# Kernel optimization log

Measured on AMD Instinct MI355X. Metric: run time of the kernel, lower is better.

## Reference

```python
import jax, jax.numpy as jnp
import numpy as np

# Model dims (see init_kwargs): embed_dim=64, heads=8, d_k = n_wires = 8
V, D, H, NQ, L, FFN = 32000, 64, 8, 8, 2, 128
B, S = 16, 1024
LAT, H1, H2, NC = 32, 128, 64, 10
INV_SQRT_DK = 1.0 / float(np.sqrt(NQ))
LN_EPS = 1e-5


def _pos_encoding(s, d):
    pos = jnp.arange(s, dtype=jnp.float32)[:, None]
    div = jnp.exp(jnp.arange(0, d, 2, dtype=jnp.float32) * (-np.log(10000.0) / d))
    pe = jnp.zeros((s, d), dtype=jnp.float32)
    pe = pe.at[:, 0::2].set(jnp.sin(pos * div))
    pe = pe.at[:, 1::2].set(jnp.cos(pos * div))
    return pe


def _layernorm(x, g, b):
    mu = jnp.mean(x, axis=-1, keepdims=True)
    var = jnp.mean(jnp.square(x - mu), axis=-1, keepdims=True)
    return (x - mu) * jax.lax.rsqrt(var + LN_EPS) * g + b


def _quantum_heads(x, theta):
    # Analytic simulation of the per-head 8-qubit VQC:
    #   RX(x_i) RX(theta_i) on wire i, CNOT ring (0->1..6->7, 7->0), measure Z.
    # Heisenberg picture: <Z_j> = prod_{i=0..j} cos(x_i+theta_i) for j>=1,
    # <Z_0> = prod_{i=1..7} cos(x_i+theta_i).
    b, s, _ = x.shape
    a = x.reshape(b, s, H, NQ) + theta            # [B,S,H,NQ]
    c = jnp.cos(a)
    cp = jnp.cumprod(c, axis=-1)
    z0 = jnp.prod(c[..., 1:], axis=-1, keepdims=True)
    return jnp.concatenate([z0, cp[..., 1:]], axis=-1)  # [B,S,H,NQ]


def _quantum_attention(x, theta, combine_W):
    qkv = _quantum_heads(x, theta)                 # [B,S,H,dk]
    q = qkv.transpose(0, 2, 1, 3)                  # [B,H,S,dk]
    scores = jnp.einsum('bhqd,bhkd->bhqk', q, q) * INV_SQRT_DK
    p = jax.nn.softmax(scores, axis=-1)
    out = jnp.einsum('bhqk,bhkd->bhqd', p, q)
    out = out.transpose(0, 2, 1, 3).reshape(x.shape[0], x.shape[1], D)
    return out @ combine_W.T                       # no bias (use_bias=False)


def _quantum_ffn(x, theta, W1, b1, W2, b2):
    # FFN QLayer: RX(x_i) then RY(theta_i), no entanglement -> <Z_i> = cos(theta_i)*cos(x_i)
    # GeneralEncoder only reads the first NQ features of each token.
    z = jnp.cos(x[..., :NQ]) * jnp.cos(theta)      # [B,S,NQ]
    h = jax.nn.relu(z @ W1.T + b1)                 # linear1 then ReLU
    return h @ W2.T + b2                           # linear2


def _forward(tokens, emb_table, attn_theta, combine_W, ln1_g, ln1_b, ln2_g, ln2_b,
             ffn_theta, ffn_W1, ffn_b1, ffn_W2, ffn_b2,
             enc_W1, enc_b1, enc_W2, enc_b2, enc_W3, enc_b3,
             dec_W1, dec_b1, dec_W2, dec_b2, dec_W3, dec_b3, cls_W, cls_b):
    x = emb_table[tokens] + _pos_encoding(tokens.shape[1], D)  # embed + positional
    for l in range(L):  # fixed small number of structurally distinct blocks
        a = _quantum_attention(x, attn_theta[l], combine_W[l])
        x = _layernorm(x + a, ln1_g[l], ln1_b[l])
        f = _quantum_ffn(x, ffn_theta[l], ffn_W1[l], ffn_b1[l], ffn_W2[l], ffn_b2[l])
        x = _layernorm(x + f, ln2_g[l], ln2_b[l])
    pooled = jnp.mean(x, axis=1)                   # [B,D]
    # AutoencoderQuantumNet.forward = decode(encode(x)) (quantum_ffn unused there)
    h = jax.nn.relu(pooled @ enc_W1.T + enc_b1)
    h = jax.nn.relu(h @ enc_W2.T + enc_b2)
    lat = h @ enc_W3.T + enc_b3
    h = jax.nn.relu(lat @ dec_W1.T + dec_b1)
    h = jax.nn.relu(h @ dec_W2.T + dec_b2)
    rec = h @ dec_W3.T + dec_b3                    # [B,D]
    return rec @ cls_W.T + cls_b                   # [B,NC]


def setup_inputs() -> dict:
    key = jax.random.key(0)
    ks = list(jax.random.split(key, 32))
    it = iter(ks)
    def nrm(shape, scale=0.05):
        return (jax.random.normal(next(it), shape) * scale).astype(jnp.float32)
    return {
        'tokens': jax.random.randint(next(it), (B, S), 0, V),
        'emb_table': nrm((V, D), 0.02),
        'attn_theta': nrm((L, NQ), 0.1),
        'combine_W': nrm((L, D, D)),
        'ln1_g': jnp.ones((L, D), jnp.float32), 'ln1_b': jnp.zeros((L, D), jnp.float32),
        'ln2_g': jnp.ones((L, D), jnp.float32), 'ln2_b': jnp.zeros((L, D), jnp.float32),
        'ffn_theta': nrm((L, NQ), 0.1),
        'ffn_W1': nrm((L, FFN, NQ)), 'ffn_b1': jnp.zeros((L, FFN), jnp.float32),
        'ffn_W2': nrm((L, D, FFN)), 'ffn_b2': jnp.zeros((L, D), jnp.float32),
        'enc_W1': nrm((H1, D)), 'enc_b1': jnp.zeros((H1,), jnp.float32),
        'enc_W2': nrm((H2, H1)), 'enc_b2': jnp.zeros((H2,), jnp.float32),
        'enc_W3': nrm((LAT, H2)), 'enc_b3': jnp.zeros((LAT,), jnp.float32),
        'dec_W1': nrm((H2, LAT)), 'dec_b1': jnp.zeros((H2,), jnp.float32),
        'dec_W2': nrm((H1, H2)), 'dec_b2': jnp.zeros((H1,), jnp.float32),
        'dec_W3': nrm((D, H1)), 'dec_b3': jnp.zeros((D,), jnp.float32),
        'cls_W': nrm((NC, D)), 'cls_b': jnp.zeros((NC,), jnp.float32),
    }


def reference(tokens, emb_table, attn_theta, combine_W, ln1_g, ln1_b, ln2_g, ln2_b,
              ffn_theta, ffn_W1, ffn_b1, ffn_W2, ffn_b2,
              enc_W1, enc_b1, enc_W2, enc_b2, enc_W3, enc_b3,
              dec_W1, dec_b1, dec_W2, dec_b2, dec_W3, dec_b3, cls_W, cls_b):
    return _forward(tokens, emb_table, attn_theta, combine_W, ln1_g, ln1_b, ln2_g, ln2_b,
                    ffn_theta, ffn_W1, ffn_b1, ffn_W2, ffn_b2,
                    enc_W1, enc_b1, enc_W2, enc_b2, enc_W3, enc_b3,
                    dec_W1, dec_b1, dec_W2, dec_b2, dec_W3, dec_b3, cls_W, cls_b)
```

## Files before the change

### kernel.cpp

```cpp
#include <hip/hip_runtime.h>
#include <math.h>

typedef _Float16 h2 __attribute__((ext_vector_type(2)));
typedef __fp16 hh4 __attribute__((ext_vector_type(4)));
typedef float f4 __attribute__((ext_vector_type(4)));

#define Bsz 16
#define Ssz 1024
#define TOKENS (Bsz * Ssz)
#define Dd 64
#define Hh 8
#define QTTS 520

#if __has_builtin(__builtin_amdgcn_exp2f)
  #define EXPFN(x) __builtin_amdgcn_exp2f(x)
  #define SQRT_PRESCALE 0.7141921f
#else
  #define EXPFN(x) __expf(x)
  #define SQRT_PRESCALE 0.5946036f
#endif

#if __has_builtin(__builtin_amdgcn_mfma_f32_16x16x16_f16)
  #define MFMA16(a, b, c) __builtin_amdgcn_mfma_f32_16x16x16_f16(a, b, c, 0, 0, 0)
#else
  #define MFMA16(a, b, c) __builtin_amdgcn_mfma_f32_16x16x16f16(a, b, c, 0, 0, 0)
#endif

__device__ __forceinline__ h2 pkrtz(float a, float b) {
#if __has_builtin(__builtin_amdgcn_cvt_pkrtz)
  return __builtin_bit_cast(h2, __builtin_amdgcn_cvt_pkrtz(a, b));
#else
  h2 r; r.x = (_Float16)a; r.y = (_Float16)b; return r;
#endif
}
__device__ __forceinline__ unsigned int as_u32(h2 v) {
  return __builtin_bit_cast(unsigned int, v);
}
__device__ __forceinline__ hh4 bc4(uint2 u) {
  return __builtin_bit_cast(hh4, u);
}

#if __has_builtin(__builtin_amdgcn_readlane)
__device__ __forceinline__ float rdlane(float v, int l) {
  return __int_as_float(__builtin_amdgcn_readlane(__float_as_int(v), l));
}
#else
__device__ __forceinline__ float rdlane(float v, int l) { return __shfl(v, l, 64); }
#endif

__device__ __forceinline__ void qheads(const float* __restrict__ xp,
                                       const float* th, float* o) {
  float4 v0 = *(const float4*)(xp);
  float4 v1 = *(const float4*)(xp + 4);
  float c0 = __cosf(v0.x + th[0]), c1 = __cosf(v0.y + th[1]);
  float c2 = __cosf(v0.z + th[2]), c3 = __cosf(v0.w + th[3]);
  float c4 = __cosf(v1.x + th[4]), c5 = __cosf(v1.y + th[5]);
  float c6 = __cosf(v1.z + th[6]), c7 = __cosf(v1.w + th[7]);
  float cp = c0;
  cp *= c1; o[1] = cp; cp *= c2; o[2] = cp; cp *= c3; o[3] = cp;
  cp *= c4; o[4] = cp; cp *= c5; o[5] = cp; cp *= c6; o[6] = cp;
  cp *= c7; o[7] = cp;
  o[0] = c1 * c2 * c3 * c4 * c5 * c6 * c7;
}

__global__ __launch_bounds__(256) void embed_kernel(
    const int* __restrict__ tokens, const float* __restrict__ emb,
    float* __restrict__ x) {
  int gid = blockIdx.x * 256 + threadIdx.x;
  if (gid >= TOKENS * 32) return;
  int d2 = gid & 31;
  int ts = gid >> 5;
  int s  = ts & (Ssz - 1);
  int tok = tokens[ts];
  float freq = __expf((float)(2 * d2) * (-0.14391156831f));
  float ang = (float)s * freq;
  float sn, cs;
  __sincosf(ang, &sn, &cs);
  float2 e2 = *(const float2*)&emb[(size_t)tok * Dd + 2 * d2];
  float2 r;
  r.x = e2.x + sn;
  r.y = e2.y + cs;
  *(float2*)&x[(size_t)ts * Dd + 2 * d2] = r;
}

__global__ __launch_bounds__(256, 4) void attn_kernel(
    const float* __restrict__ x, const float* __restrict__ theta,
    float* __restrict__ o_out, float* __restrict__ ps_out) {
  __shared__ unsigned int qrs[Ssz * 4 + 2];
  __shared__ unsigned int qtt[8 * QTTS];
  int blk = blockIdx.x;
  int bh = blk >> 3, split = blk & 7;
  int b = bh >> 3, h = bh & 7;
  int t = threadIdx.x;

  float th[8];
#pragma unroll
  for (int i = 0; i < 8; i++) th[i] = theta[i];

  const float* xb = x + (size_t)b * Ssz * Dd + h * 8;

#pragma unroll
  for (int i = 0; i < 4; i += 2) {
    int k0 = t * 4 + i;
    float oa[8], ob[8];
    qheads(xb + (size_t)k0 * Dd, th, oa);
    qheads(xb + (size_t)(k0 + 1) * Dd, th, ob);
    uint4 wa, wb;
    wa.x = as_u32(pkrtz(oa[0] * SQRT_PRESCALE, oa[1] * SQRT_PRESCALE));
    wa.y = as_u32(pkrtz(oa[2] * SQRT_PRESCALE, oa[3] * SQRT_PRESCALE));
    wa.z = as_u32(pkrtz(oa[4] * SQRT_PRESCALE, oa[5] * SQRT_PRESCALE));
    wa.w = as_u32(pkrtz(oa[6] * SQRT_PRESCALE, oa[7] * SQRT_PRESCALE));
    wb.x = as_u32(pkrtz(ob[0] * SQRT_PRESCALE, ob[1] * SQRT_PRESCALE));
    wb.y = as_u32(pkrtz(ob[2] * SQRT_PRESCALE, ob[3] * SQRT_PRESCALE));
    wb.z = as_u32(pkrtz(ob[4] * SQRT_PRESCALE, ob[5] * SQRT_PRESCALE));
    wb.w = as_u32(pkrtz(ob[6] * SQRT_PRESCALE, ob[7] * SQRT_PRESCALE));
    *(uint4*)&qrs[k0 * 4] = wa;
    *(uint4*)&qrs[(k0 + 1) * 4] = wb;
#pragma unroll
    for (int d = 0; d < 8; d++)
      qtt[d * QTTS + (k0 >> 1)] = as_u32(pkrtz(oa[d], ob[d]));
  }
  if (t == 0) { qrs[Ssz * 4] = 0; qrs[Ssz * 4 + 1] = 0; }
  __syncthreads();

  int l = t & 63, w = t >> 6;
  int g = l >> 4, rr = l & 15;
  int rt0 = split * 8 + w * 2;
  int rowA = rt0 * 16 + rr;
  int rowB = rowA + 16;
  uint2 z2; z2.x = 0; z2.y = 0;
  uint2 buA = (g < 2) ? *(const uint2*)&qrs[rowA * 4 + 2 * g] : z2;
  uint2 buB = (g < 2) ? *(const uint2*)&qrs[rowB * 4 + 2 * g] : z2;
  hh4 BrA = bc4(buA), BrB = bc4(buB);
  int aoff  = (g < 2) ? (rr * 4 + 2 * g) : (Ssz * 4);
  int astep = (g < 2) ? 64 : 0;
  int qoff  = (rr & 7) * QTTS + 2 * g;
  f4 zf = {0.f, 0.f, 0.f, 0.f};
  f4 accA0 = zf, accB0 = zf, accA1 = zf, accB1 = zf;
  float psA0 = 0.f, psB0 = 0.f, psA1 = 0.f, psB1 = 0.f;

#pragma unroll 4
  for (int kt = 0; kt < 64; kt += 2) {
    {
      uint2 au = *(const uint2*)&qrs[aoff + kt * astep];
      hh4 Ak = bc4(au);
      f4 sA = MFMA16(Ak, BrA, zf);
      f4 sB = MFMA16(Ak, BrB, zf);
      float pA0 = EXPFN(sA.x), pA1 = EXPFN(sA.y), pA2 = EXPFN(sA.z), pA3 = EXPFN(sA.w);
      float pB0 = EXPFN(sB.x), pB1 = EXPFN(sB.y), pB2 = EXPFN(sB.z), pB3 = EXPFN(sB.w);
      psA0 += (pA0 + pA1) + (pA2 + pA3);
      psB0 += (pB0 + pB1) + (pB2 + pB3);
      uint2 pbA, pbB;
      pbA.x = as_u32(pkrtz(pA0, pA1)); pbA.y = as_u32(pkrtz(pA2, pA3));
      pbB.x = as_u32(pkrtz(pB0, pB1)); pbB.y = as_u32(pkrtz(pB2, pB3));
      uint2 qt = *(const uint2*)&qtt[qoff + kt * 8];
      hh4 Aq = bc4(qt);
      accA0 = MFMA16(Aq, bc4(pbA), accA0);
      accB0 = MFMA16(Aq, bc4(pbB), accB0);
    }
    {
      uint2 au = *(const uint2*)&qrs[aoff + (kt + 1) * astep];
      hh4 Ak = bc4(au);
      f4 sA = MFMA16(Ak, BrA, zf);
      f4 sB = MFMA16(Ak, BrB, zf);
      float pA0 = EXPFN(sA.x), pA1 = EXPFN(sA.y), pA2 = EXPFN(sA.z), pA3 = EXPFN(sA.w);
      float pB0 = EXPFN(sB.x), pB1 = EXPFN(sB.y), pB2 = EXPFN(sB.z), pB3 = EXPFN(sB.w);
      psA1 += (pA0 + pA1) + (pA2 + pA3);
      psB1 += (pB0 + pB1) + (pB2 + pB3);
      uint2 pbA, pbB;
      pbA.x = as_u32(pkrtz(pA0, pA1)); pbA.y = as_u32(pkrtz(pA2, pA3));
      pbB.x = as_u32(pkrtz(pB0, pB1)); pbB.y = as_u32(pkrtz(pB2, pB3));
      uint2 qt = *(const uint2*)&qtt[qoff + (kt + 1) * 8];
      hh4 Aq = bc4(qt);
      accA1 = MFMA16(Aq, bc4(pbA), accA1);
      accB1 = MFMA16(Aq, bc4(pbB), accB1);
    }
  }
  f4 accA = accA0 + accA1;
  f4 accB = accB0 + accB1;
  float psA = psA0 + psA1, psB = psB0 + psB1;
  psA += __shfl_xor(psA, 16, 64); psA += __shfl_xor(psA, 32, 64);
  psB += __shfl_xor(psB, 16, 64); psB += __shfl_xor(psB, 32, 64);

  size_t tokA = (size_t)b * Ssz + rowA;
  size_t tokB = (size_t)b * Ssz + rowB;
  if (g < 2) {
    *(f4*)&o_out[tokA * 64 + h * 8 + 4 * g] = accA;
    *(f4*)&o_out[tokB * 64 + h * 8 + 4 * g] = accB;
  }
  if (l < 16) {
    ps_out[tokA * 8 + h] = psA;
    ps_out[tokB * 8 + h] = psB;
  }
}

__global__ __launch_bounds__(64) void tail1_kernel(
    float* __restrict__ x, const float* __restrict__ o_out,
    const float* __restrict__ ps_out, const float* __restrict__ Wc,
    const float* __restrict__ g1, const float* __restrict__ bb1) {
  int l = threadIdx.x & 63;
  int g = l >> 4, c = l & 15;
  int tok0 = blockIdx.x * 16;

  hh4 Bf[4][4];
#pragma unroll
  for (int dc = 0; dc < 4; dc++)
#pragma unroll
    for (int kc = 0; kc < 4; kc++) {
      float4 wv = *(const float4*)&Wc[(size_t)(dc * 16 + c) * 64 + kc * 16 + 4 * g];
      uint2 u; u.x = as_u32(pkrtz(wv.x, wv.y)); u.y = as_u32(pkrtz(wv.z, wv.w));
      Bf[kc][dc] = bc4(u);
    }

  int tka = tok0 + c;
  hh4 Af[4];
#pragma unroll
  for (int kc = 0; kc < 4; kc++) {
    float4 o4 = *(const float4*)&o_out[(size_t)tka * 64 + kc * 16 + 4 * g];
    float inv = 1.0f / ps_out[(size_t)tka * 8 + kc * 2 + (g >> 1)];
    uint2 u;
    u.x = as_u32(pkrtz(o4.x * inv, o4.y * inv));
    u.y = as_u32(pkrtz(o4.z * inv, o4.w * inv));
    Af[kc] = bc4(u);
  }

  f4 zf = {0.f, 0.f, 0.f, 0.f};
  float yy[4][4];
#pragma unroll
  for (int dc = 0; dc < 4; dc++) {
    f4 acc = zf;
#pragma unroll
    for (int kc = 0; kc < 4; kc++) acc = MFMA16(Af[kc], Bf[kc][dc], acc);
    yy[dc][0] = acc.x; yy[dc][1] = acc.y; yy[dc][2] = acc.z; yy[dc][3] = acc.w;
  }

  float g1v[4], b1v[4];
#pragma unroll
  for (int dc = 0; dc < 4; dc++) { g1v[dc] = g1[dc * 16 + c]; b1v[dc] = bb1[dc * 16 + c]; }

#pragma unroll
  for (int r = 0; r < 4; r++) {
    int tok = tok0 + 4 * g + r;
    float rv0 = x[(size_t)tok * 64 + c]      + yy[0][r];
    float rv1 = x[(size_t)tok * 64 + 16 + c] + yy[1][r];
    float rv2 = x[(size_t)tok * 64 + 32 + c] + yy[2][r];
    float rv3 = x[(size_t)tok * 64 + 48 + c] + yy[3][r];
    float s = (rv0 + rv1) + (rv2 + rv3);
    s += __shfl_xor(s, 1, 64); s += __shfl_xor(s, 2, 64);
    s += __shfl_xor(s, 4, 64); s += __shfl_xor(s, 8, 64);
    float mu = s * (1.f / 64.f);
    float t0 = rv0 - mu, t1 = rv1 - mu, t2 = rv2 - mu, t3 = rv3 - mu;
    float q = (t0 * t0 + t1 * t1) + (t2 * t2 + t3 * t3);
    q += __shfl_xor(q, 1, 64); q += __shfl_xor(q, 2, 64);
    q += __shfl_xor(q, 4, 64); q += __shfl_xor(q, 8, 64);
    float inv = rsqrtf(q * (1.f / 64.f) + 1e-5f);
    x[(size_t)tok * 64 + c]      = t0 * inv * g1v[0] + b1v[0];
    x[(size_t)tok * 64 + 16 + c] = t1 * inv * g1v[1] + b1v[1];
    x[(size_t)tok * 64 + 32 + c] = t2 * inv * g1v[2] + b1v[2];
    x[(size_t)tok * 64 + 48 + c] = t3 * inv * g1v[3] + b1v[3];
  }
}

__global__ __launch_bounds__(64) void tail2_kernel(
    float* __restrict__ x,
    const float* __restrict__ g2, const float* __restrict__ bb2,
    const float* __restrict__ fth,
    const float* __restrict__ W1, const float* __restrict__ fb1,
    const float* __restrict__ W2, const float* __restrict__ fb2,
    float* __restrict__ partial, int do_partial) {
  int l = threadIdx.x & 63;
  int g = l >> 4, c = l & 15;
  int tok0 = blockIdx.x * 16;

  float4 x4[4];
#pragma unroll
  for (int dc = 0; dc < 4; dc++)
    x4[dc] = *(const float4*)&x[(size_t)(tok0 + c) * 64 + dc * 16 + 4 * g];

  uint2 uz; uz.x = 0; uz.y = 0;
  if (g < 2) {
    float4 thv = *(const float4*)&fth[4 * g];
    float z0 = __cosf(x4[0].x) * __cosf(thv.x);
    float z1 = __cosf(x4[0].y) * __cosf(thv.y);
    float z2 = __cosf(x4[0].z) * __cosf(thv.z);
    float z3 = __cosf(x4[0].w) * __cosf(thv.w);
    uz.x = as_u32(pkrtz(z0, z1)); uz.y = as_u32(pkrtz(z2, z3));
  }
  hh4 Bz = bc4(uz);

  f4 zf = {0.f, 0.f, 0.f, 0.f};

  hh4 Bh[8];
#pragma unroll
  for (int jc = 0; jc < 8; jc++) {
    uint2 uw; uw.x = 0; uw.y = 0;
    if (g < 2) {
      float4 wv = *(const float4*)&W1[(size_t)(jc * 16 + c) * 8 + 4 * g];
      uw.x = as_u32(pkrtz(wv.x, wv.y)); uw.y = as_u32(pkrtz(wv.z, wv.w));
    }
    f4 d1 = MFMA16(bc4(uw), Bz, zf);
    float4 b1v = *(const float4*)&fb1[jc * 16 + 4 * g];
    float h0 = fmaxf(d1.x + b1v.x, 0.f);
    float h1 = fmaxf(d1.y + b1v.y, 0.f);
    float h2 = fmaxf(d1.z + b1v.z, 0.f);
    float h3 = fmaxf(d1.w + b1v.w, 0.f);
    uint2 uh;
    uh.x = as_u32(pkrtz(h0, h1)); uh.y = as_u32(pkrtz(h2, h3));
    Bh[jc] = bc4(uh);
  }

  float ff[4][4];
#pragma unroll
  for (int dc = 0; dc < 4; dc++) {
    f4 acc = zf;
#pragma unroll
    for (int kc = 0; kc < 8; kc++) {
      float4 wv = *(const float4*)&W2[(size_t)(dc * 16 + c) * 128 + kc * 16 + 4 * g];
      uint2 uw;
      uw.x = as_u32(pkrtz(wv.x, wv.y)); uw.y = as_u32(pkrtz(wv.z, wv.w));
      acc = MFMA16(bc4(uw), Bh[kc], acc);
    }
    ff[dc][0] = acc.x; ff[dc][1] = acc.y; ff[dc][2] = acc.z; ff[dc][3] = acc.w;
  }

  float r2[4][4];
  float s = 0.f;
#pragma unroll
  for (int dc = 0; dc < 4; dc++) {
    float4 b2v = *(const float4*)&fb2[dc * 16 + 4 * g];
    r2[dc][0] = x4[dc].x + ff[dc][0] + b2v.x;
    r2[dc][1] = x4[dc].y + ff[dc][1] + b2v.y;
    r2[dc][2] = x4[dc].z + ff[dc][2] + b2v.z;
    r2[dc][3] = x4[dc].w + ff[dc][3] + b2v.w;
    s += (r2[dc][0] + r2[dc][1]) + (r2[dc][2] + r2[dc][3]);
  }
  s += __shfl_xor(s, 16, 64); s += __shfl_xor(s, 32, 64);
  float mu = s * (1.f / 64.f);
  float q = 0.f;
#pragma unroll
  for (int dc = 0; dc < 4; dc++) {
#pragma unroll
    for (int r = 0; r < 4; r++) { r2[dc][r] -= mu; q += r2[dc][r] * r2[dc][r]; }
  }
  q += __shfl_xor(q, 16, 64); q += __shfl_xor(q, 32, 64);
  float inv = rsqrtf(q * (1.f / 64.f) + 1e-5f);

  float xo[4][4];
#pragma unroll
  for (int dc = 0; dc < 4; dc++) {
    float4 gv = *(const float4*)&g2[dc * 16 + 4 * g];
    float4 bv = *(const float4*)&bb2[dc * 16 + 4 * g];
    xo[dc][0] = r2[dc][0] * inv * gv.x + bv.x;
    xo[dc][1] = r2[dc][1] * inv * gv.y + bv.y;
    xo[dc][2] = r2[dc][2] * inv * gv.z + bv.z;
    xo[dc][3] = r2[dc][3] * inv * gv.w + bv.w;
    float4 o4;
    o4.x = xo[dc][0]; o4.y = xo[dc][1]; o4.z = xo[dc][2]; o4.w = xo[dc][3];
    *(float4*)&x[(size_t)(tok0 + c) * 64 + dc * 16 + 4 * g] = o4;
  }

  if (do_partial) {
#pragma unroll
    for (int dc = 0; dc < 4; dc++)
#pragma unroll
      for (int r = 0; r < 4; r++) {
        float p = xo[dc][r];
        p += __shfl_xor(p, 1, 64); p += __shfl_xor(p, 2, 64);
        p += __shfl_xor(p, 4, 64); p += __shfl_xor(p, 8, 64);
        xo[dc][r] = p;
      }
    if (c == 0) {
#pragma unroll
      for (int dc = 0; dc < 4; dc++) {
        float4 o4;
        o4.x = xo[dc][0]; o4.y = xo[dc][1]; o4.z = xo[dc][2]; o4.w = xo[dc][3];
        *(float4*)&partial[(size_t)blockIdx.x * 64 + dc * 16 + 4 * g] = o4;
      }
    }
  }
}

__global__ __launch_bounds__(128) void head_kernel(
    const float* __restrict__ partial,
    const float* eW1, const float* eb1, const float* eW2, const float* eb2,
    const float* eW3, const float* eb3, const float* dW1, const float* db1v,
    const float* dW2, const float* db2v, const float* dW3, const float* db3v,
    const float* cW, const float* cb, float* __restrict__ out) {
  __shared__ float bufP[64];
  __shared__ float bufA[128];
  __shared__ float bufB[128];
  int b = blockIdx.x, t = threadIdx.x;
  if (t < 64) {
    float s = 0.f;
    for (int c = 0; c < 64; ++c) s += partial[(size_t)(b * 64 + c) * 64 + t];
    bufP[t] = s * (1.f / 1024.f);
  }
  __syncthreads();
  {
    float v = eb1[t];
    for (int d = 0; d < 64; d++) v = fmaf(bufP[d], eW1[t * 64 + d], v);
    bufA[t] = fmaxf(v, 0.f);
  }
  __syncthreads();
  if (t < 64) {
    float v = eb2[t];
    for (int j = 0; j < 128; j++) v = fmaf(bufA[j], eW2[t * 128 + j], v);
    bufB[t] = fmaxf(v, 0.f);
  }
  __syncthreads();
  if (t < 32) {
    float v = eb3[t];
    for (int d = 0; d < 64; d++) v = fmaf(bufB[d], eW3[t * 64 + d], v);
    bufA[t] = v;
  }
  __syncthreads();
  if (t < 64) {
    float v = db1v[t];
    for (int k = 0; k < 32; k++) v = fmaf(bufA[k], dW1[t * 32 + k], v);
    bufB[t] = fmaxf(v, 0.f);
  }
  __syncthreads();
  {
    float v = db2v[t];
    for (int k = 0; k < 64; k++) v = fmaf(bufB[k], dW2[t * 64 + k], v);
    bufA[t] = fmaxf(v, 0.f);
  }
  __syncthreads();
  if (t < 64) {
    float v = db3v[t];
    for (int j = 0; j < 128; j++) v = fmaf(bufA[j], dW3[t * 128 + j], v);
    bufB[t] = v;
  }
  __syncthreads();
  if (t < 10) {
    float v = cb[t];
    for (int d = 0; d < 64; d++) v = fmaf(bufB[d], cW[t * 64 + d], v);
    out[b * 10 + t] = v;
  }
}

extern "C" void kernel_launch(void* const* d_in, const int* in_sizes, int n_in,
                              void* d_out, int out_size, void* d_ws, size_t ws_size,
                              hipStream_t stream) {
  const int*   tokens     = (const int*)d_in[0];
  const float* emb        = (const float*)d_in[1];
  const float* attn_theta = (const float*)d_in[2];
  const float* combine_W  = (const float*)d_in[3];
  const float* ln1_g      = (const float*)d_in[4];
  const float* ln1_b      = (const float*)d_in[5];
  const float* ln2_g      = (const float*)d_in[6];
  const float* ln2_b      = (const float*)d_in[7];
  const float* ffn_theta  = (const float*)d_in[8];
  const float* ffn_W1     = (const float*)d_in[9];
  const float* ffn_b1     = (const float*)d_in[10];
  const float* ffn_W2     = (const float*)d_in[11];
  const float* ffn_b2     = (const float*)d_in[12];
  const float* enc_W1 = (const float*)d_in[13]; const float* enc_b1 = (const float*)d_in[14];
  const float* enc_W2 = (const float*)d_in[15]; const float* enc_b2 = (const float*)d_in[16];
  const float* enc_W3 = (const float*)d_in[17]; const float* enc_b3 = (const float*)d_in[18];
  const float* dec_W1 = (const float*)d_in[19]; const float* dec_b1 = (const float*)d_in[20];
  const float* dec_W2 = (const float*)d_in[21]; const float* dec_b2 = (const float*)d_in[22];
  const float* dec_W3 = (const float*)d_in[23]; const float* dec_b3 = (const float*)d_in[24];
  const float* cls_W  = (const float*)d_in[25]; const float* cls_b  = (const float*)d_in[26];

  float* x       = (float*)d_ws;
  float* o_out   = x + (size_t)TOKENS * 64;
  float* ps_out  = o_out + (size_t)TOKENS * 64;
  float* partial = ps_out + (size_t)TOKENS * 8;
  float* out     = (float*)d_out;

  embed_kernel<<<(TOKENS * 32 + 255) / 256, 256, 0, stream>>>(tokens, emb, x);
  for (int l = 0; l < 2; ++l) {
    attn_kernel<<<128 * 8, 256, 0, stream>>>(x, attn_theta + l * 8, o_out, ps_out);
    tail1_kernel<<<TOKENS / 16, 64, 0, stream>>>(
        x, o_out, ps_out, combine_W + l * 4096, ln1_g + l * 64, ln1_b + l * 64);
    tail2_kernel<<<TOKENS / 16, 64, 0, stream>>>(
        x, ln2_g + l * 64, ln2_b + l * 64,
        ffn_theta + l * 8, ffn_W1 + l * 1024, ffn_b1 + l * 128,
        ffn_W2 + l * 8192, ffn_b2 + l * 64, partial, (l == 1) ? 1 : 0);
  }
  head_kernel<<<16, 128, 0, stream>>>(partial, enc_W1, enc_b1, enc_W2, enc_b2,
                                      enc_W3, enc_b3, dec_W1, dec_b1, dec_W2,
                                      dec_b2, dec_W3, dec_b3, cls_W, cls_b, out);
}
```

Measured before the change: 102.3 us.

## Fold softmax row sums into MFMA via ones row and fuse tail kernels

The attention kernel drops its explicit per-lane exp-sum accumulation and shuffle reduction. Instead it adds a ninth row of fp16 ones to the transposed Q tile, so the existing P·V MFMA also yields the softmax denominator in an otherwise unused output row. Separately, the combine/LayerNorm1 tail and the FFN/LayerNorm2 tail become one kernel that keeps the normalized activations in shared memory, saving a launch and a global round trip of x. The denominator is now accumulated from fp16-rounded probabilities, which may slightly change accuracy.

```diff
diff --git a/kernel.cpp b/kernel.cpp
--- a/kernel.cpp
+++ b/kernel.cpp
@@ -39,14 +39,6 @@
 __device__ __forceinline__ hh4 bc4(uint2 u) {
   return __builtin_bit_cast(hh4, u);
 }
-
-#if __has_builtin(__builtin_amdgcn_readlane)
-__device__ __forceinline__ float rdlane(float v, int l) {
-  return __int_as_float(__builtin_amdgcn_readlane(__float_as_int(v), l));
-}
-#else
-__device__ __forceinline__ float rdlane(float v, int l) { return __shfl(v, l, 64); }
-#endif
 
 __device__ __forceinline__ void qheads(const float* __restrict__ xp,
                                        const float* th, float* o) {
@@ -87,7 +79,7 @@
     const float* __restrict__ x, const float* __restrict__ theta,
     float* __restrict__ o_out, float* __restrict__ ps_out) {
   __shared__ unsigned int qrs[Ssz * 4 + 2];
-  __shared__ unsigned int qtt[8 * QTTS];
+  __shared__ unsigned int qtt[9 * QTTS];
   int blk = blockIdx.x;
   int bh = blk >> 3, split = blk & 7;
   int b = bh >> 3, h = bh & 7;
@@ -120,6 +112,7 @@
     for (int d = 0; d < 8; d++)
       qtt[d * QTTS + (k0 >> 1)] = as_u32(pkrtz(oa[d], ob[d]));
   }
+  for (int j = 8 * QTTS + t; j < 9 * QTTS; j += 256) qtt[j] = 0x3C003C00u;
   if (t == 0) { qrs[Ssz * 4] = 0; qrs[Ssz * 4 + 1] = 0; }
   __syncthreads();
 
@@ -134,10 +127,10 @@
   hh4 BrA = bc4(buA), BrB = bc4(buB);
   int aoff  = (g < 2) ? (rr * 4 + 2 * g) : (Ssz * 4);
   int astep = (g < 2) ? 64 : 0;
-  int qoff  = (rr & 7) * QTTS + 2 * g;
+  int qrow  = (rr >= 8) ? 8 : rr;
+  int qoff  = qrow * QTTS + 2 * g;
   f4 zf = {0.f, 0.f, 0.f, 0.f};
   f4 accA0 = zf, accB0 = zf, accA1 = zf, accB1 = zf;
-  float psA0 = 0.f, psB0 = 0.f, psA1 = 0.f, psB1 = 0.f;
 
 #pragma unroll 4
   for (int kt = 0; kt < 64; kt += 2) {
@@ -148,8 +141,6 @@
       f4 sB = MFMA16(Ak, BrB, zf);
       float pA0 = EXPFN(sA.x), pA1 = EXPFN(sA.y), pA2 = EXPFN(sA.z), pA3 = EXPFN(sA.w);
       float pB0 = EXPFN(sB.x), pB1 = EXPFN(sB.y), pB2 = EXPFN(sB.z), pB3 = EXPFN(sB.w);
-      psA0 += (pA0 + pA1) + (pA2 + pA3);
-      psB0 += (pB0 + pB1) + (pB2 + pB3);
       uint2 pbA, pbB;
       pbA.x = as_u32(pkrtz(pA0, pA1)); pbA.y = as_u32(pkrtz(pA2, pA3));
       pbB.x = as_u32(pkrtz(pB0, pB1)); pbB.y = as_u32(pkrtz(pB2, pB3));
@@ -165,8 +156,6 @@
       f4 sB = MFMA16(Ak, BrB, zf);
       float pA0 = EXPFN(sA.x), pA1 = EXPFN(sA.y), pA2 = EXPFN(sA.z), pA3 = EXPFN(sA.w);
       float pB0 = EXPFN(sB.x), pB1 = EXPFN(sB.y), pB2 = EXPFN(sB.z), pB3 = EXPFN(sB.w);
-      psA1 += (pA0 + pA1) + (pA2 + pA3);
-      psB1 += (pB0 + pB1) + (pB2 + pB3);
       uint2 pbA, pbB;
       pbA.x = as_u32(pkrtz(pA0, pA1)); pbA.y = as_u32(pkrtz(pA2, pA3));
       pbB.x = as_u32(pkrtz(pB0, pB1)); pbB.y = as_u32(pkrtz(pB2, pB3));
@@ -178,104 +167,93 @@
   }
   f4 accA = accA0 + accA1;
   f4 accB = accB0 + accB1;
-  float psA = psA0 + psA1, psB = psB0 + psB1;
-  psA += __shfl_xor(psA, 16, 64); psA += __shfl_xor(psA, 32, 64);
-  psB += __shfl_xor(psB, 16, 64); psB += __shfl_xor(psB, 32, 64);
 
   size_t tokA = (size_t)b * Ssz + rowA;
   size_t tokB = (size_t)b * Ssz + rowB;
   if (g < 2) {
     *(f4*)&o_out[tokA * 64 + h * 8 + 4 * g] = accA;
     *(f4*)&o_out[tokB * 64 + h * 8 + 4 * g] = accB;
-  }
-  if (l < 16) {
-    ps_out[tokA * 8 + h] = psA;
-    ps_out[tokB * 8 + h] = psB;
-  }
-}
-
-__global__ __launch_bounds__(64) void tail1_kernel(
+  } else if (g == 2) {
+    ps_out[tokA * 8 + h] = accA.x;
+    ps_out[tokB * 8 + h] = accB.x;
+  }
+}
+
+__global__ __launch_bounds__(64) void tail_kernel(
     float* __restrict__ x, const float* __restrict__ o_out,
     const float* __restrict__ ps_out, const float* __restrict__ Wc,
-    const float* __restrict__ g1, const float* __restrict__ bb1) {
-  int l = threadIdx.x & 63;
-  int g = l >> 4, c = l & 15;
-  int tok0 = blockIdx.x * 16;
-
-  hh4 Bf[4][4];
-#pragma unroll
-  for (int dc = 0; dc < 4; dc++)
-#pragma unroll
-    for (int kc = 0; kc < 4; kc++) {
-      float4 wv = *(const float4*)&Wc[(size_t)(dc * 16 + c) * 64 + kc * 16 + 4 * g];
-      uint2 u; u.x = as_u32(pkrtz(wv.x, wv.y)); u.y = as_u32(pkrtz(wv.z, wv.w));
-      Bf[kc][dc] = bc4(u);
-    }
-
-  int tka = tok0 + c;
-  hh4 Af[4];
-#pragma unroll
-  for (int kc = 0; kc < 4; kc++) {
-    float4 o4 = *(const float4*)&o_out[(size_t)tka * 64 + kc * 16 + 4 * g];
-    float inv = 1.0f / ps_out[(size_t)tka * 8 + kc * 2 + (g >> 1)];
-    uint2 u;
-    u.x = as_u32(pkrtz(o4.x * inv, o4.y * inv));
-    u.y = as_u32(pkrtz(o4.z * inv, o4.w * inv));
-    Af[kc] = bc4(u);
-  }
-
-  f4 zf = {0.f, 0.f, 0.f, 0.f};
-  float yy[4][4];
-#pragma unroll
-  for (int dc = 0; dc < 4; dc++) {
-    f4 acc = zf;
-#pragma unroll
-    for (int kc = 0; kc < 4; kc++) acc = MFMA16(Af[kc], Bf[kc][dc], acc);
-    yy[dc][0] = acc.x; yy[dc][1] = acc.y; yy[dc][2] = acc.z; yy[dc][3] = acc.w;
-  }
-
-  float g1v[4], b1v[4];
-#pragma unroll
-  for (int dc = 0; dc < 4; dc++) { g1v[dc] = g1[dc * 16 + c]; b1v[dc] = bb1[dc * 16 + c]; }
-
-#pragma unroll
-  for (int r = 0; r < 4; r++) {
-    int tok = tok0 + 4 * g + r;
-    float rv0 = x[(size_t)tok * 64 + c]      + yy[0][r];
-    float rv1 = x[(size_t)tok * 64 + 16 + c] + yy[1][r];
-    float rv2 = x[(size_t)tok * 64 + 32 + c] + yy[2][r];
-    float rv3 = x[(size_t)tok * 64 + 48 + c] + yy[3][r];
-    float s = (rv0 + rv1) + (rv2 + rv3);
-    s += __shfl_xor(s, 1, 64); s += __shfl_xor(s, 2, 64);
-    s += __shfl_xor(s, 4, 64); s += __shfl_xor(s, 8, 64);
-    float mu = s * (1.f / 64.f);
-    float t0 = rv0 - mu, t1 = rv1 - mu, t2 = rv2 - mu, t3 = rv3 - mu;
-    float q = (t0 * t0 + t1 * t1) + (t2 * t2 + t3 * t3);
-    q += __shfl_xor(q, 1, 64); q += __shfl_xor(q, 2, 64);
-    q += __shfl_xor(q, 4, 64); q += __shfl_xor(q, 8, 64);
-    float inv = rsqrtf(q * (1.f / 64.f) + 1e-5f);
-    x[(size_t)tok * 64 + c]      = t0 * inv * g1v[0] + b1v[0];
-    x[(size_t)tok * 64 + 16 + c] = t1 * inv * g1v[1] + b1v[1];
-    x[(size_t)tok * 64 + 32 + c] = t2 * inv * g1v[2] + b1v[2];
-    x[(size_t)tok * 64 + 48 + c] = t3 * inv * g1v[3] + b1v[3];
-  }
-}
-
-__global__ __launch_bounds__(64) void tail2_kernel(
-    float* __restrict__ x,
+    const float* __restrict__ g1, const float* __restrict__ bb1,
     const float* __restrict__ g2, const float* __restrict__ bb2,
     const float* __restrict__ fth,
     const float* __restrict__ W1, const float* __restrict__ fb1,
     const float* __restrict__ W2, const float* __restrict__ fb2,
     float* __restrict__ partial, int do_partial) {
+  __shared__ float xbuf[16][68];
   int l = threadIdx.x & 63;
   int g = l >> 4, c = l & 15;
   int tok0 = blockIdx.x * 16;
+  f4 zf = {0.f, 0.f, 0.f, 0.f};
+
+  {
+    hh4 Bf[4][4];
+#pragma unroll
+    for (int dc = 0; dc < 4; dc++)
+#pragma unroll
+      for (int kc = 0; kc < 4; kc++) {
+        float4 wv = *(const float4*)&Wc[(size_t)(dc * 16 + c) * 64 + kc * 16 + 4 * g];
+        uint2 u; u.x = as_u32(pkrtz(wv.x, wv.y)); u.y = as_u32(pkrtz(wv.z, wv.w));
+        Bf[kc][dc] = bc4(u);
+      }
+    int tka = tok0 + c;
+    hh4 Af[4];
+#pragma unroll
+    for (int kc = 0; kc < 4; kc++) {
+      float4 o4 = *(const float4*)&o_out[(size_t)tka * 64 + kc * 16 + 4 * g];
+      float inv = 1.0f / ps_out[(size_t)tka * 8 + kc * 2 + (g >> 1)];
+      uint2 u;
+      u.x = as_u32(pkrtz(o4.x * inv, o4.y * inv));
+      u.y = as_u32(pkrtz(o4.z * inv, o4.w * inv));
+      Af[kc] = bc4(u);
+    }
+    float yy[4][4];
+#pragma unroll
+    for (int dc = 0; dc < 4; dc++) {
+      f4 acc = zf;
+#pragma unroll
+      for (int kc = 0; kc < 4; kc++) acc = MFMA16(Af[kc], Bf[kc][dc], acc);
+      yy[dc][0] = acc.x; yy[dc][1] = acc.y; yy[dc][2] = acc.z; yy[dc][3] = acc.w;
+    }
+    float g1v[4], b1v[4];
+#pragma unroll
+    for (int dc = 0; dc < 4; dc++) { g1v[dc] = g1[dc * 16 + c]; b1v[dc] = bb1[dc * 16 + c]; }
+#pragma unroll
+    for (int r = 0; r < 4; r++) {
+      int tok = tok0 + 4 * g + r;
+      float rv0 = x[(size_t)tok * 64 + c]      + yy[0][r];
+      float rv1 = x[(size_t)tok * 64 + 16 + c] + yy[1][r];
+      float rv2 = x[(size_t)tok * 64 + 32 + c] + yy[2][r];
+      float rv3 = x[(size_t)tok * 64 + 48 + c] + yy[3][r];
+      float s = (rv0 + rv1) + (rv2 + rv3);
+      s += __shfl_xor(s, 1, 64); s += __shfl_xor(s, 2, 64);
+      s += __shfl_xor(s, 4, 64); s += __shfl_xor(s, 8, 64);
+      float mu = s * (1.f / 64.f);
+      float t0 = rv0 - mu, t1 = rv1 - mu, t2 = rv2 - mu, t3 = rv3 - mu;
+      float q = (t0 * t0 + t1 * t1) + (t2 * t2 + t3 * t3);
+      q += __shfl_xor(q, 1, 64); q += __shfl_xor(q, 2, 64);
+      q += __shfl_xor(q, 4, 64); q += __shfl_xor(q, 8, 64);
+      float inv = rsqrtf(q * (1.f / 64.f) + 1e-5f);
+      int tk = 4 * g + r;
+      xbuf[tk][c]      = t0 * inv * g1v[0] + b1v[0];
+      xbuf[tk][16 + c] = t1 * inv * g1v[1] + b1v[1];
+      xbuf[tk][32 + c] = t2 * inv * g1v[2] + b1v[2];
+      xbuf[tk][48 + c] = t3 * inv * g1v[3] + b1v[3];
+    }
+  }
 
   float4 x4[4];
 #pragma unroll
   for (int dc = 0; dc < 4; dc++)
-    x4[dc] = *(const float4*)&x[(size_t)(tok0 + c) * 64 + dc * 16 + 4 * g];
+    x4[dc] = *(const float4*)&xbuf[c][dc * 16 + 4 * g];
 
   uint2 uz; uz.x = 0; uz.y = 0;
   if (g < 2) {
@@ -287,8 +265,6 @@
     uz.x = as_u32(pkrtz(z0, z1)); uz.y = as_u32(pkrtz(z2, z3));
   }
   hh4 Bz = bc4(uz);
-
-  f4 zf = {0.f, 0.f, 0.f, 0.f};
 
   hh4 Bh[8];
 #pragma unroll
@@ -472,10 +448,9 @@
   embed_kernel<<<(TOKENS * 32 + 255) / 256, 256, 0, stream>>>(tokens, emb, x);
   for (int l = 0; l < 2; ++l) {
     attn_kernel<<<128 * 8, 256, 0, stream>>>(x, attn_theta + l * 8, o_out, ps_out);
-    tail1_kernel<<<TOKENS / 16, 64, 0, stream>>>(
-        x, o_out, ps_out, combine_W + l * 4096, ln1_g + l * 64, ln1_b + l * 64);
-    tail2_kernel<<<TOKENS / 16, 64, 0, stream>>>(
-        x, ln2_g + l * 64, ln2_b + l * 64,
+    tail_kernel<<<TOKENS / 16, 64, 0, stream>>>(
+        x, o_out, ps_out, combine_W + l * 4096,
+        ln1_g + l * 64, ln1_b + l * 64, ln2_g + l * 64, ln2_b + l * 64,
         ffn_theta + l * 8, ffn_W1 + l * 1024, ffn_b1 + l * 128,
         ffn_W2 + l * 8192, ffn_b2 + l * 64, partial, (l == 1) ? 1 : 0);
   }
```

Result: faster. 89.91 us (-12.1%).
